# Kernel tuning notes

Hardware: AMD Instinct MI355X
Metric: run time of the kernel (lower is better)

## Reference

```python
import jax, jax.numpy as jnp
import numpy as np

STEP_SIZE = 0.3333
MAX_STEPS = 8          # >= ceil(max(2*sigma)/step); extra iterations have k==0 (no-op)
TANGENT_DIRECTION = True


def _bilinear_sample(img, p):
    # img: [B,C,H,W], p: [B,2,H,W] normalized coords in [0,1] (x=width, y=height)
    B, C, H, W = img.shape
    fx = p[:, 0] * W - 0.5   # [B,H,W] pixel-center convention
    fy = p[:, 1] * H - 0.5
    x0 = jnp.floor(fx)
    y0 = jnp.floor(fy)
    wx = (fx - x0)[:, None]  # [B,1,H,W]
    wy = (fy - y0)[:, None]
    x0i = jnp.clip(x0.astype(jnp.int32), 0, W - 1)
    x1i = jnp.clip(x0i + 1, 0, W - 1)
    y0i = jnp.clip(y0.astype(jnp.int32), 0, H - 1)
    y1i = jnp.clip(y0i + 1, 0, H - 1)
    gather = jax.vmap(lambda im, yi, xi: im[:, yi, xi])  # per-batch gather -> [B,C,H,W]
    v00 = gather(img, y0i, x0i)
    v01 = gather(img, y0i, x1i)
    v10 = gather(img, y1i, x0i)
    v11 = gather(img, y1i, x1i)
    return (v00 * (1 - wx) + v01 * wx) * (1 - wy) + (v10 * (1 - wx) + v11 * wx) * wy


def _p_start(H, W, dtype):
    xs = (jnp.arange(W, dtype=dtype) + 0.5) / W
    ys = (jnp.arange(H, dtype=dtype) + 0.5) / H
    px = jnp.broadcast_to(xs[None, :], (H, W))
    py = jnp.broadcast_to(ys[:, None], (H, W))
    return jnp.stack([px, py])[None]  # [1,2,H,W]


def _perp(t):
    return jnp.concatenate([t[:, 1:2], -t[:, 0:1]], axis=1)


def _forward(x, tangent, sigma):
    B, C, H, W = x.shape
    dt = x.dtype
    factor = min(H, W) / 1024.0          # input_size_factor relative to 1024 base res
    sigma = sigma * factor               # [B,1,1,1]
    half_width = 2.0 * sigma
    two_sigma2 = 2.0 * sigma * sigma
    step = jnp.asarray(1.0 / (STEP_SIZE * factor), dtype=dt)
    tex = jnp.array([W, H], dtype=dt).reshape(1, 2, 1, 1)
    p0 = _p_start(H, W, dt)

    def one_pass(direction):
        v = direction if TANGENT_DIRECTION else _perp(direction)
        p = p0 + v / tex
        r = jnp.broadcast_to(step, (B, 1, 1, 1))
        c = jnp.zeros_like(x)
        s = jnp.zeros((B, 1, H, W), dt)

        def body(carry, _):
            c, s, v, p, r = carry
            k = jnp.exp(-r * r / two_sigma2)                 # [B,1,1,1]
            k = jnp.where(r < half_width, k, 0.0)
            inb = ((p[:, 0:1] >= 0.0) & (p[:, 0:1] < 1.0) &
                   (p[:, 1:2] >= 0.0) & (p[:, 1:2] < 1.0))   # [B,1,H,W]
            k = jnp.where(inb, k, 0.0)                        # [B,1,H,W]
            c = c + _bilinear_sample(x, p) * k
            s = s + k
            tf = _bilinear_sample(tangent, p)                 # [B,2,H,W]
            if not TANGENT_DIRECTION:
                tf = _perp(tf)
            vt = jnp.sum(v * tf, axis=1, keepdims=True)
            tf = jnp.where(vt < 0.0, -tf, tf)                 # keep marching direction coherent
            return (c, s, tf, p + tf / tex, r + step), None

        (c, s, _, _, _), _ = jax.lax.scan(body, (c, s, v, p, r), None, length=MAX_STEPS)
        return c, s

    c1, s1 = one_pass(tangent)
    c2, s2 = one_pass(-tangent)
    return (x + c1 + c2) / (1.0 + s1 + s2)


def setup_inputs() -> dict:
    key = jax.random.key(0)
    k1, k2, k3 = jax.random.split(key, 3)
    B, C, H, W = 2, 3, 1024, 1024
    x = jax.random.uniform(k1, (B, C, H, W), dtype=jnp.float32)
    t = jax.random.normal(k2, (B, 2, H, W), dtype=jnp.float32)
    t = t / (jnp.sqrt(jnp.sum(t * t, axis=1, keepdims=True)) + 1e-6)  # unit tangent field
    sigma = 2.0 + 4.0 * jax.random.uniform(k3, (B, 1, 1, 1), dtype=jnp.float32)
    return {"x": x, "tangent": t, "sigma": sigma}


def reference(x, tangent, sigma):
    return _forward(x, tangent, sigma)
```

## Files before the change

kernel.cpp:

```cpp
#include <hip/hip_runtime.h>
#include <hip/hip_fp16.h>


#define HH 1024
#define WW 1024
#define CC 3
#define BB 2
#define NPIX (HH * WW)

#define TSX 16
#define TSY 16
#define HALO_LO 4
#define NWIN 25

__device__ __forceinline__ float uaf(unsigned u) { return __uint_as_float(u); }
__device__ __forceinline__ __half2 h2(unsigned u) {
    __half2 r; *(unsigned*)&r = u; return r;
}

__global__ __launch_bounds__(256) void flow_smooth_lds(
    const float* __restrict__ x, const float* __restrict__ tng,
    const float* __restrict__ sigma, float* __restrict__ out)
{
    __shared__ float2 tanw[NWIN * NWIN];
    __shared__ uint2  colw[NWIN * NWIN];

    const int id  = (int)blockIdx.x + ((int)blockIdx.y << 6) + ((int)blockIdx.z << 12);
    const int swz = ((id & 7) << 10) + (id >> 3);
    const int bx = swz & 63;
    const int by = (swz >> 6) & 63;
    const int b  = swz >> 12;

    const int tile_x0 = bx * TSX;
    const int tile_y0 = by * TSY;
    const int win_x0 = tile_x0 - HALO_LO;
    const int win_y0 = tile_y0 - HALO_LO;
    const bool border = (bx == 0) | (bx == 63) | (by == 0) | (by == 63);

    const float* __restrict__ xb  = x   + (size_t)b * CC * NPIX;
    const float* __restrict__ tbx = tng + (size_t)b * 2 * NPIX;
    const float* __restrict__ tby = tbx + NPIX;

    if (!border) {
        const int gbase = win_y0 * WW + win_x0;
        for (unsigned j = threadIdx.x; j < NWIN * NWIN; j += 256) {
            const int jy = (int)(j / NWIN);
            const int jx = (int)j - jy * NWIN;
            const int g = gbase + (jy << 10) + jx;
            tanw[j] = make_float2(tbx[g], tby[g]);
            const __half2 c01 = __floats2half2_rn(xb[g], xb[NPIX + g]);
            const __half2 c2p = __floats2half2_rn(xb[2 * NPIX + g], 0.f);
            uint2 r;
            r.x = *(const unsigned*)&c01;
            r.y = *(const unsigned*)&c2p;
            colw[j] = r;
        }
    } else {
        for (unsigned j = threadIdx.x; j < NWIN * NWIN; j += 256) {
            const int jy = (int)(j / NWIN);
            const int jx = (int)j - jy * NWIN;
            const int gy = min(max(win_y0 + jy, 0), HH - 1);
            const int gx = min(max(win_x0 + jx, 0), WW - 1);
            const int g = gy * WW + gx;
            tanw[j] = make_float2(tbx[g], tby[g]);
            const __half2 c01 = __floats2half2_rn(xb[g], xb[NPIX + g]);
            const __half2 c2p = __floats2half2_rn(xb[2 * NPIX + g], 0.f);
            uint2 r;
            r.x = *(const unsigned*)&c01;
            r.y = *(const unsigned*)&c2p;
            colw[j] = r;
        }
    }
    __syncthreads();

    const int tx = threadIdx.x & (TSX - 1);
    const int ty = threadIdx.x >> 4;
    const int ix = tile_x0 + tx;
    const int iy = tile_y0 + ty;
    const int pix = iy * WW + ix;

    const float sig = sigma[b];
    const float half_width = 2.0f * sig;
    const float inv2s2 = 1.0f / (2.0f * sig * sig);
    const float step = (float)(1.0 / 0.3333);

    const float r0 = step;
    const float r1 = r0 + step;
    const float r2 = r1 + step;
    const int nlive = (int)(r0 < half_width) + (int)(r1 < half_width) + (int)(r2 < half_width);
    const float kk0 = __expf(-r0 * r0 * inv2s2);
    const float kk1 = __expf(-r1 * r1 * inv2s2);
    const float kk2 = __expf(-r2 * r2 * inv2s2);

    const float xc0 = xb[pix];
    const float xc1 = xb[NPIX + pix];
    const float xc2 = xb[2 * NPIX + pix];
    const int cidx = (ty + HALO_LO) * NWIN + (tx + HALO_LO);
    const float2 tc = tanw[cidx];
    const float t0x = tc.x;
    const float t0y = tc.y;

    const float invW = 1.0f / WW;
    const float invH = 1.0f / HH;

    float acc0 = 0.f, acc1 = 0.f, acc2 = 0.f, accs = 0.f;

    float vx[2], vy[2], px[2], py[2];
    vx[0] = t0x;  vy[0] = t0y;
    vx[1] = -t0x; vy[1] = -t0y;
    const float p0x = ((float)ix + 0.5f) * invW;
    const float p0y = ((float)iy + 0.5f) * invH;
    px[0] = p0x + vx[0] * invW;  py[0] = p0y + vy[0] * invH;
    px[1] = p0x + vx[1] * invW;  py[1] = p0y + vy[1] * invH;

    if (!border) {
        const int winoff = win_y0 * NWIN + win_x0;
        #pragma unroll
        for (int it = 0; it < 3; ++it) {
            if (it >= nlive) break;
            const float k = (it == 0) ? kk0 : (it == 1) ? kk1 : kk2;
            const bool need_t = (it + 1 < nlive);
            #pragma unroll
            for (int c = 0; c < 2; ++c) {
                const float fx = fmaf(px[c], (float)WW, -0.5f);
                const float fy = fmaf(py[c], (float)HH, -0.5f);
                const float x0f = floorf(fx);
                const float y0f = floorf(fy);
                const float wx = fx - x0f;
                const float wy = fy - y0f;
                const int idx = (int)y0f * NWIN + (int)x0f - winoff;

                const float wxm = 1.f - wx, wym = 1.f - wy;
                const float w00 = wxm * wym, w01 = wx * wym;
                const float w10 = wxm * wy,  w11 = wx * wy;

                const uint2 q00 = colw[idx];
                const uint2 q01 = colw[idx + 1];
                const uint2 q10 = colw[idx + NWIN];
                const uint2 q11 = colw[idx + NWIN + 1];
                const __half2 h00 = __float2half2_rn(w00);
                const __half2 h01 = __float2half2_rn(w01);
                const __half2 h10 = __float2half2_rn(w10);
                const __half2 h11 = __float2half2_rn(w11);
                __half2 a01 = __hmul2(h00, h2(q00.x));
                a01 = __hfma2(h01, h2(q01.x), a01);
                a01 = __hfma2(h10, h2(q10.x), a01);
                a01 = __hfma2(h11, h2(q11.x), a01);
                __half2 a2 = __hmul2(h00, h2(q00.y));
                a2 = __hfma2(h01, h2(q01.y), a2);
                a2 = __hfma2(h10, h2(q10.y), a2);
                a2 = __hfma2(h11, h2(q11.y), a2);
                acc0 = fmaf(k, __low2float(a01), acc0);
                acc1 = fmaf(k, __high2float(a01), acc1);
                acc2 = fmaf(k, __low2float(a2), acc2);

                if (need_t) {
                    const float2 t00 = tanw[idx];
                    const float2 t01 = tanw[idx + 1];
                    const float2 t10 = tanw[idx + NWIN];
                    const float2 t11 = tanw[idx + NWIN + 1];
                    float tfx = t00.x * w00 + t01.x * w01 + t10.x * w10 + t11.x * w11;
                    float tfy = t00.y * w00 + t01.y * w01 + t10.y * w10 + t11.y * w11;
                    const float vt = vx[c] * tfx + vy[c] * tfy;
                    const unsigned sgn = __float_as_uint(vt) & 0x80000000u;
                    tfx = __uint_as_float(__float_as_uint(tfx) ^ sgn);
                    tfy = __uint_as_float(__float_as_uint(tfy) ^ sgn);
                    vx[c] = tfx; vy[c] = tfy;
                    px[c] += tfx * invW;
                    py[c] += tfy * invH;
                }
            }
        }
        float ks = 0.f;
        if (nlive > 0) ks += kk0;
        if (nlive > 1) ks += kk1;
        if (nlive > 2) ks += kk2;
        accs = 2.0f * ks;
    } else {
        #pragma unroll
        for (int it = 0; it < 3; ++it) {
            if (it >= nlive) break;
            const float k = (it == 0) ? kk0 : (it == 1) ? kk1 : kk2;
            #pragma unroll
            for (int c = 0; c < 2; ++c) {
                const float fx = fmaf(px[c], (float)WW, -0.5f);
                const float fy = fmaf(py[c], (float)HH, -0.5f);
                const float x0f = floorf(fx);
                const float y0f = floorf(fy);
                const float wx = fx - x0f;
                const float wy = fy - y0f;
                int x0i = (int)x0f;
                int y0i = (int)y0f;
                x0i = min(max(x0i, 0), WW - 1);
                y0i = min(max(y0i, 0), HH - 1);
                const int x1i = min(x0i + 1, WW - 1);
                const int y1i = min(y0i + 1, HH - 1);

                const int jx0 = x0i - win_x0;
                const int jx1 = x1i - win_x0;
                const int jy0 = y0i - win_y0;
                const int jy1 = y1i - win_y0;
                const int i00 = jy0 * NWIN + jx0;
                const int i01 = jy0 * NWIN + jx1;
                const int i10 = jy1 * NWIN + jx0;
                const int i11 = jy1 * NWIN + jx1;

                const float wxm = 1.f - wx, wym = 1.f - wy;
                const float w00 = wxm * wym, w01 = wx * wym;
                const float w10 = wxm * wy,  w11 = wx * wy;

                const bool inb = (px[c] >= 0.f) & (px[c] < 1.f) &
                                 (py[c] >= 0.f) & (py[c] < 1.f);
                const float kg = inb ? k : 0.f;

                const uint2 q00 = colw[i00];
                const uint2 q01 = colw[i01];
                const uint2 q10 = colw[i10];
                const uint2 q11 = colw[i11];
                const __half2 h00 = __float2half2_rn(w00);
                const __half2 h01 = __float2half2_rn(w01);
                const __half2 h10 = __float2half2_rn(w10);
                const __half2 h11 = __float2half2_rn(w11);
                __half2 a01 = __hmul2(h00, h2(q00.x));
                a01 = __hfma2(h01, h2(q01.x), a01);
                a01 = __hfma2(h10, h2(q10.x), a01);
                a01 = __hfma2(h11, h2(q11.x), a01);
                __half2 a2 = __hmul2(h00, h2(q00.y));
                a2 = __hfma2(h01, h2(q01.y), a2);
                a2 = __hfma2(h10, h2(q10.y), a2);
                a2 = __hfma2(h11, h2(q11.y), a2);
                acc0 = fmaf(kg, __low2float(a01), acc0);
                acc1 = fmaf(kg, __high2float(a01), acc1);
                acc2 = fmaf(kg, __low2float(a2), acc2);
                accs += kg;

                const float2 t00 = tanw[i00];
                const float2 t01 = tanw[i01];
                const float2 t10 = tanw[i10];
                const float2 t11 = tanw[i11];
                float tfx = t00.x * w00 + t01.x * w01 + t10.x * w10 + t11.x * w11;
                float tfy = t00.y * w00 + t01.y * w01 + t10.y * w10 + t11.y * w11;
                const float vt = vx[c] * tfx + vy[c] * tfy;
                const unsigned sgn = __float_as_uint(vt) & 0x80000000u;
                tfx = __uint_as_float(__float_as_uint(tfx) ^ sgn);
                tfy = __uint_as_float(__float_as_uint(tfy) ^ sgn);
                vx[c] = tfx; vy[c] = tfy;
                px[c] += tfx * invW;
                py[c] += tfy * invH;
            }
        }
    }

    const float inv_den = 1.0f / (1.0f + accs);
    float* ob = out + (size_t)b * CC * NPIX;
    ob[pix]            = (xc0 + acc0) * inv_den;
    ob[NPIX + pix]     = (xc1 + acc1) * inv_den;
    ob[2 * NPIX + pix] = (xc2 + acc2) * inv_den;
}

extern "C" void kernel_launch(void* const* d_in, const int* in_sizes, int n_in,
                              void* d_out, int out_size, void* d_ws, size_t ws_size,
                              hipStream_t stream) {
    const float* x  = (const float*)d_in[0];
    const float* t  = (const float*)d_in[1];
    const float* sg = (const float*)d_in[2];
    float* out = (float*)d_out;

    dim3 grid(WW / TSX, HH / TSY, BB);
    flow_smooth_lds<<<grid, dim3(256), 0, stream>>>(x, t, sg, out);
}
```

Measured before the change: 108.4 us.

## Widen tile to 32x16 with two pixels per thread to cut halo overhead

Each 256-thread block now covers a 32x16 tile, with every thread handling two pixels 16 columns apart. The shared window becomes 41x25 instead of 25x25, which lowers the halo load cost per output pixel and halves the block count. In exchange each thread holds more registers and the block uses more LDS, which may reduce occupancy. Each thread also has two independent chains, giving more instruction-level parallelism.

```diff
diff --git a/kernel.cpp b/kernel.cpp
--- a/kernel.cpp
+++ b/kernel.cpp
@@ -8,12 +8,13 @@
 #define BB 2
 #define NPIX (HH * WW)
 
-#define TSX 16
+#define TSX 32
 #define TSY 16
 #define HALO_LO 4
-#define NWIN 25
-
-__device__ __forceinline__ float uaf(unsigned u) { return __uint_as_float(u); }
+#define NWX 41
+#define NWY 25
+#define NREC (NWX * NWY)
+
 __device__ __forceinline__ __half2 h2(unsigned u) {
     __half2 r; *(unsigned*)&r = u; return r;
 }
@@ -22,20 +23,20 @@
     const float* __restrict__ x, const float* __restrict__ tng,
     const float* __restrict__ sigma, float* __restrict__ out)
 {
-    __shared__ float2 tanw[NWIN * NWIN];
-    __shared__ uint2  colw[NWIN * NWIN];
-
-    const int id  = (int)blockIdx.x + ((int)blockIdx.y << 6) + ((int)blockIdx.z << 12);
-    const int swz = ((id & 7) << 10) + (id >> 3);
-    const int bx = swz & 63;
-    const int by = (swz >> 6) & 63;
-    const int b  = swz >> 12;
+    __shared__ float2 tanw[NREC];
+    __shared__ uint2  colw[NREC];
+
+    const int id  = (int)blockIdx.x + ((int)blockIdx.y << 5) + ((int)blockIdx.z << 11);
+    const int swz = ((id & 7) << 9) + (id >> 3);
+    const int bx = swz & 31;
+    const int by = (swz >> 5) & 63;
+    const int b  = swz >> 11;
 
     const int tile_x0 = bx * TSX;
     const int tile_y0 = by * TSY;
     const int win_x0 = tile_x0 - HALO_LO;
     const int win_y0 = tile_y0 - HALO_LO;
-    const bool border = (bx == 0) | (bx == 63) | (by == 0) | (by == 63);
+    const bool border = (bx == 0) | (bx == 31) | (by == 0) | (by == 63);
 
     const float* __restrict__ xb  = x   + (size_t)b * CC * NPIX;
     const float* __restrict__ tbx = tng + (size_t)b * 2 * NPIX;
@@ -43,9 +44,9 @@
 
     if (!border) {
         const int gbase = win_y0 * WW + win_x0;
-        for (unsigned j = threadIdx.x; j < NWIN * NWIN; j += 256) {
-            const int jy = (int)(j / NWIN);
-            const int jx = (int)j - jy * NWIN;
+        for (unsigned j = threadIdx.x; j < NREC; j += 256) {
+            const int jy = (int)(j / NWX);
+            const int jx = (int)j - jy * NWX;
             const int g = gbase + (jy << 10) + jx;
             tanw[j] = make_float2(tbx[g], tby[g]);
             const __half2 c01 = __floats2half2_rn(xb[g], xb[NPIX + g]);
@@ -56,9 +57,9 @@
             colw[j] = r;
         }
     } else {
-        for (unsigned j = threadIdx.x; j < NWIN * NWIN; j += 256) {
-            const int jy = (int)(j / NWIN);
-            const int jx = (int)j - jy * NWIN;
+        for (unsigned j = threadIdx.x; j < NREC; j += 256) {
+            const int jy = (int)(j / NWX);
+            const int jx = (int)j - jy * NWX;
             const int gy = min(max(win_y0 + jy, 0), HH - 1);
             const int gx = min(max(win_x0 + jx, 0), WW - 1);
             const int g = gy * WW + gx;
@@ -73,11 +74,9 @@
     }
     __syncthreads();
 
-    const int tx = threadIdx.x & (TSX - 1);
+    const int tx = threadIdx.x & 15;
     const int ty = threadIdx.x >> 4;
-    const int ix = tile_x0 + tx;
     const int iy = tile_y0 + ty;
-    const int pix = iy * WW + ix;
 
     const float sig = sigma[b];
     const float half_width = 2.0f * sig;
@@ -92,82 +91,90 @@
     const float kk1 = __expf(-r1 * r1 * inv2s2);
     const float kk2 = __expf(-r2 * r2 * inv2s2);
 
-    const float xc0 = xb[pix];
-    const float xc1 = xb[NPIX + pix];
-    const float xc2 = xb[2 * NPIX + pix];
-    const int cidx = (ty + HALO_LO) * NWIN + (tx + HALO_LO);
-    const float2 tc = tanw[cidx];
-    const float t0x = tc.x;
-    const float t0y = tc.y;
-
     const float invW = 1.0f / WW;
     const float invH = 1.0f / HH;
 
-    float acc0 = 0.f, acc1 = 0.f, acc2 = 0.f, accs = 0.f;
-
-    float vx[2], vy[2], px[2], py[2];
-    vx[0] = t0x;  vy[0] = t0y;
-    vx[1] = -t0x; vy[1] = -t0y;
-    const float p0x = ((float)ix + 0.5f) * invW;
-    const float p0y = ((float)iy + 0.5f) * invH;
-    px[0] = p0x + vx[0] * invW;  py[0] = p0y + vy[0] * invH;
-    px[1] = p0x + vx[1] * invW;  py[1] = p0y + vy[1] * invH;
+    int   ix[2], pix[2];
+    float xc0[2], xc1[2], xc2[2];
+    float acc0[2] = {0.f, 0.f}, acc1[2] = {0.f, 0.f};
+    float acc2[2] = {0.f, 0.f}, accs[2] = {0.f, 0.f};
+    float vx[2][2], vy[2][2], px[2][2], py[2][2];
+
+    #pragma unroll
+    for (int pp = 0; pp < 2; ++pp) {
+        ix[pp] = tile_x0 + tx + pp * 16;
+        pix[pp] = iy * WW + ix[pp];
+        xc0[pp] = xb[pix[pp]];
+        xc1[pp] = xb[NPIX + pix[pp]];
+        xc2[pp] = xb[2 * NPIX + pix[pp]];
+        const int cidx = (ty + HALO_LO) * NWX + (tx + pp * 16 + HALO_LO);
+        const float2 tc = tanw[cidx];
+        vx[pp][0] = tc.x;  vy[pp][0] = tc.y;
+        vx[pp][1] = -tc.x; vy[pp][1] = -tc.y;
+        const float p0x = ((float)ix[pp] + 0.5f) * invW;
+        const float p0y = ((float)iy + 0.5f) * invH;
+        px[pp][0] = p0x + vx[pp][0] * invW;  py[pp][0] = p0y + vy[pp][0] * invH;
+        px[pp][1] = p0x + vx[pp][1] * invW;  py[pp][1] = p0y + vy[pp][1] * invH;
+    }
 
     if (!border) {
-        const int winoff = win_y0 * NWIN + win_x0;
+        const int winoff = win_y0 * NWX + win_x0;
         #pragma unroll
         for (int it = 0; it < 3; ++it) {
             if (it >= nlive) break;
             const float k = (it == 0) ? kk0 : (it == 1) ? kk1 : kk2;
             const bool need_t = (it + 1 < nlive);
             #pragma unroll
-            for (int c = 0; c < 2; ++c) {
-                const float fx = fmaf(px[c], (float)WW, -0.5f);
-                const float fy = fmaf(py[c], (float)HH, -0.5f);
-                const float x0f = floorf(fx);
-                const float y0f = floorf(fy);
-                const float wx = fx - x0f;
-                const float wy = fy - y0f;
-                const int idx = (int)y0f * NWIN + (int)x0f - winoff;
-
-                const float wxm = 1.f - wx, wym = 1.f - wy;
-                const float w00 = wxm * wym, w01 = wx * wym;
-                const float w10 = wxm * wy,  w11 = wx * wy;
-
-                const uint2 q00 = colw[idx];
-                const uint2 q01 = colw[idx + 1];
-                const uint2 q10 = colw[idx + NWIN];
-                const uint2 q11 = colw[idx + NWIN + 1];
-                const __half2 h00 = __float2half2_rn(w00);
-                const __half2 h01 = __float2half2_rn(w01);
-                const __half2 h10 = __float2half2_rn(w10);
-                const __half2 h11 = __float2half2_rn(w11);
-                __half2 a01 = __hmul2(h00, h2(q00.x));
-                a01 = __hfma2(h01, h2(q01.x), a01);
-                a01 = __hfma2(h10, h2(q10.x), a01);
-                a01 = __hfma2(h11, h2(q11.x), a01);
-                __half2 a2 = __hmul2(h00, h2(q00.y));
-                a2 = __hfma2(h01, h2(q01.y), a2);
-                a2 = __hfma2(h10, h2(q10.y), a2);
-                a2 = __hfma2(h11, h2(q11.y), a2);
-                acc0 = fmaf(k, __low2float(a01), acc0);
-                acc1 = fmaf(k, __high2float(a01), acc1);
-                acc2 = fmaf(k, __low2float(a2), acc2);
-
-                if (need_t) {
-                    const float2 t00 = tanw[idx];
-                    const float2 t01 = tanw[idx + 1];
-                    const float2 t10 = tanw[idx + NWIN];
-                    const float2 t11 = tanw[idx + NWIN + 1];
-                    float tfx = t00.x * w00 + t01.x * w01 + t10.x * w10 + t11.x * w11;
-                    float tfy = t00.y * w00 + t01.y * w01 + t10.y * w10 + t11.y * w11;
-                    const float vt = vx[c] * tfx + vy[c] * tfy;
-                    const unsigned sgn = __float_as_uint(vt) & 0x80000000u;
-                    tfx = __uint_as_float(__float_as_uint(tfx) ^ sgn);
-                    tfy = __uint_as_float(__float_as_uint(tfy) ^ sgn);
-                    vx[c] = tfx; vy[c] = tfy;
-                    px[c] += tfx * invW;
-                    py[c] += tfy * invH;
+            for (int pp = 0; pp < 2; ++pp) {
+                #pragma unroll
+                for (int c = 0; c < 2; ++c) {
+                    const float fx = fmaf(px[pp][c], (float)WW, -0.5f);
+                    const float fy = fmaf(py[pp][c], (float)HH, -0.5f);
+                    const float x0f = floorf(fx);
+                    const float y0f = floorf(fy);
+                    const float wx = fx - x0f;
+                    const float wy = fy - y0f;
+                    const int idx = (int)y0f * NWX + (int)x0f - winoff;
+
+                    const float wxm = 1.f - wx, wym = 1.f - wy;
+                    const float w00 = wxm * wym, w01 = wx * wym;
+                    const float w10 = wxm * wy,  w11 = wx * wy;
+
+                    const uint2 q00 = colw[idx];
+                    const uint2 q01 = colw[idx + 1];
+                    const uint2 q10 = colw[idx + NWX];
+                    const uint2 q11 = colw[idx + NWX + 1];
+                    const __half2 h00 = __float2half2_rn(w00);
+                    const __half2 h01 = __float2half2_rn(w01);
+                    const __half2 h10 = __float2half2_rn(w10);
+                    const __half2 h11 = __float2half2_rn(w11);
+                    __half2 a01 = __hmul2(h00, h2(q00.x));
+                    a01 = __hfma2(h01, h2(q01.x), a01);
+                    a01 = __hfma2(h10, h2(q10.x), a01);
+                    a01 = __hfma2(h11, h2(q11.x), a01);
+                    __half2 a2 = __hmul2(h00, h2(q00.y));
+                    a2 = __hfma2(h01, h2(q01.y), a2);
+                    a2 = __hfma2(h10, h2(q10.y), a2);
+                    a2 = __hfma2(h11, h2(q11.y), a2);
+                    acc0[pp] = fmaf(k, __low2float(a01), acc0[pp]);
+                    acc1[pp] = fmaf(k, __high2float(a01), acc1[pp]);
+                    acc2[pp] = fmaf(k, __low2float(a2), acc2[pp]);
+
+                    if (need_t) {
+                        const float2 t00 = tanw[idx];
+                        const float2 t01 = tanw[idx + 1];
+                        const float2 t10 = tanw[idx + NWX];
+                        const float2 t11 = tanw[idx + NWX + 1];
+                        float tfx = t00.x * w00 + t01.x * w01 + t10.x * w10 + t11.x * w11;
+                        float tfy = t00.y * w00 + t01.y * w01 + t10.y * w10 + t11.y * w11;
+                        const float vt = vx[pp][c] * tfx + vy[pp][c] * tfy;
+                        const unsigned sgn = __float_as_uint(vt) & 0x80000000u;
+                        tfx = __uint_as_float(__float_as_uint(tfx) ^ sgn);
+                        tfy = __uint_as_float(__float_as_uint(tfy) ^ sgn);
+                        vx[pp][c] = tfx; vy[pp][c] = tfy;
+                        px[pp][c] += tfx * invW;
+                        py[pp][c] += tfy * invH;
+                    }
                 }
             }
         }
@@ -175,87 +182,94 @@
         if (nlive > 0) ks += kk0;
         if (nlive > 1) ks += kk1;
         if (nlive > 2) ks += kk2;
-        accs = 2.0f * ks;
+        accs[0] = 2.0f * ks;
+        accs[1] = accs[0];
     } else {
         #pragma unroll
         for (int it = 0; it < 3; ++it) {
             if (it >= nlive) break;
             const float k = (it == 0) ? kk0 : (it == 1) ? kk1 : kk2;
             #pragma unroll
-            for (int c = 0; c < 2; ++c) {
-                const float fx = fmaf(px[c], (float)WW, -0.5f);
-                const float fy = fmaf(py[c], (float)HH, -0.5f);
-                const float x0f = floorf(fx);
-                const float y0f = floorf(fy);
-                const float wx = fx - x0f;
-                const float wy = fy - y0f;
-                int x0i = (int)x0f;
-                int y0i = (int)y0f;
-                x0i = min(max(x0i, 0), WW - 1);
-                y0i = min(max(y0i, 0), HH - 1);
-                const int x1i = min(x0i + 1, WW - 1);
-                const int y1i = min(y0i + 1, HH - 1);
-
-                const int jx0 = x0i - win_x0;
-                const int jx1 = x1i - win_x0;
-                const int jy0 = y0i - win_y0;
-                const int jy1 = y1i - win_y0;
-                const int i00 = jy0 * NWIN + jx0;
-                const int i01 = jy0 * NWIN + jx1;
-                const int i10 = jy1 * NWIN + jx0;
-                const int i11 = jy1 * NWIN + jx1;
-
-                const float wxm = 1.f - wx, wym = 1.f - wy;
-                const float w00 = wxm * wym, w01 = wx * wym;
-                const float w10 = wxm * wy,  w11 = wx * wy;
-
-                const bool inb = (px[c] >= 0.f) & (px[c] < 1.f) &
-                                 (py[c] >= 0.f) & (py[c] < 1.f);
-                const float kg = inb ? k : 0.f;
-
-                const uint2 q00 = colw[i00];
-                const uint2 q01 = colw[i01];
-                const uint2 q10 = colw[i10];
-                const uint2 q11 = colw[i11];
-                const __half2 h00 = __float2half2_rn(w00);
-                const __half2 h01 = __float2half2_rn(w01);
-                const __half2 h10 = __float2half2_rn(w10);
-                const __half2 h11 = __float2half2_rn(w11);
-                __half2 a01 = __hmul2(h00, h2(q00.x));
-                a01 = __hfma2(h01, h2(q01.x), a01);
-                a01 = __hfma2(h10, h2(q10.x), a01);
-                a01 = __hfma2(h11, h2(q11.x), a01);
-                __half2 a2 = __hmul2(h00, h2(q00.y));
-                a2 = __hfma2(h01, h2(q01.y), a2);
-                a2 = __hfma2(h10, h2(q10.y), a2);
-                a2 = __hfma2(h11, h2(q11.y), a2);
-                acc0 = fmaf(kg, __low2float(a01), acc0);
-                acc1 = fmaf(kg, __high2float(a01), acc1);
-                acc2 = fmaf(kg, __low2float(a2), acc2);
-                accs += kg;
-
-                const float2 t00 = tanw[i00];
-                const float2 t01 = tanw[i01];
-                const float2 t10 = tanw[i10];
-                const float2 t11 = tanw[i11];
-                float tfx = t00.x * w00 + t01.x * w01 + t10.x * w10 + t11.x * w11;
-                float tfy = t00.y * w00 + t01.y * w01 + t10.y * w10 + t11.y * w11;
-                const float vt = vx[c] * tfx + vy[c] * tfy;
-                const unsigned sgn = __float_as_uint(vt) & 0x80000000u;
-                tfx = __uint_as_float(__float_as_uint(tfx) ^ sgn);
-                tfy = __uint_as_float(__float_as_uint(tfy) ^ sgn);
-                vx[c] = tfx; vy[c] = tfy;
-                px[c] += tfx * invW;
-                py[c] += tfy * invH;
+            for (int pp = 0; pp < 2; ++pp) {
+                #pragma unroll
+                for (int c = 0; c < 2; ++c) {
+                    const float fx = fmaf(px[pp][c], (float)WW, -0.5f);
+                    const float fy = fmaf(py[pp][c], (float)HH, -0.5f);
+                    const float x0f = floorf(fx);
+                    const float y0f = floorf(fy);
+                    const float wx = fx - x0f;
+                    const float wy = fy - y0f;
+                    int x0i = (int)x0f;
+                    int y0i = (int)y0f;
+                    x0i = min(max(x0i, 0), WW - 1);
+                    y0i = min(max(y0i, 0), HH - 1);
+                    const int x1i = min(x0i + 1, WW - 1);
+                    const int y1i = min(y0i + 1, HH - 1);
+
+                    const int jx0 = x0i - win_x0;
+                    const int jx1 = x1i - win_x0;
+                    const int jy0 = y0i - win_y0;
+                    const int jy1 = y1i - win_y0;
+                    const int i00 = jy0 * NWX + jx0;
+                    const int i01 = jy0 * NWX + jx1;
+                    const int i10 = jy1 * NWX + jx0;
+                    const int i11 = jy1 * NWX + jx1;
+
+                    const float wxm = 1.f - wx, wym = 1.f - wy;
+                    const float w00 = wxm * wym, w01 = wx * wym;
+                    const float w10 = wxm * wy,  w11 = wx * wy;
+
+                    const bool inb = (px[pp][c] >= 0.f) & (px[pp][c] < 1.f) &
+                                     (py[pp][c] >= 0.f) & (py[pp][c] < 1.f);
+                    const float kg = inb ? k : 0.f;
+
+                    const uint2 q00 = colw[i00];
+                    const uint2 q01 = colw[i01];
+                    const uint2 q10 = colw[i10];
+                    const uint2 q11 = colw[i11];
+                    const __half2 h00 = __float2half2_rn(w00);
+                    const __half2 h01 = __float2half2_rn(w01);
+                    const __half2 h10 = __float2half2_rn(w10);
+                    const __half2 h11 = __float2half2_rn(w11);
+                    __half2 a01 = __hmul2(h00, h2(q00.x));
+                    a01 = __hfma2(h01, h2(q01.x), a01);
+                    a01 = __hfma2(h10, h2(q10.x), a01);
+                    a01 = __hfma2(h11, h2(q11.x), a01);
+                    __half2 a2 = __hmul2(h00, h2(q00.y));
+                    a2 = __hfma2(h01, h2(q01.y), a2);
+                    a2 = __hfma2(h10, h2(q10.y), a2);
+                    a2 = __hfma2(h11, h2(q11.y), a2);
+                    acc0[pp] = fmaf(kg, __low2float(a01), acc0[pp]);
+                    acc1[pp] = fmaf(kg, __high2float(a01), acc1[pp]);
+                    acc2[pp] = fmaf(kg, __low2float(a2), acc2[pp]);
+                    accs[pp] += kg;
+
+                    const float2 t00 = tanw[i00];
+                    const float2 t01 = tanw[i01];
+                    const float2 t10 = tanw[i10];
+                    const float2 t11 = tanw[i11];
+                    float tfx = t00.x * w00 + t01.x * w01 + t10.x * w10 + t11.x * w11;
+                    float tfy = t00.y * w00 + t01.y * w01 + t10.y * w10 + t11.y * w11;
+                    const float vt = vx[pp][c] * tfx + vy[pp][c] * tfy;
+                    const unsigned sgn = __float_as_uint(vt) & 0x80000000u;
+                    tfx = __uint_as_float(__float_as_uint(tfx) ^ sgn);
+                    tfy = __uint_as_float(__float_as_uint(tfy) ^ sgn);
+                    vx[pp][c] = tfx; vy[pp][c] = tfy;
+                    px[pp][c] += tfx * invW;
+                    py[pp][c] += tfy * invH;
+                }
             }
         }
     }
 
-    const float inv_den = 1.0f / (1.0f + accs);
     float* ob = out + (size_t)b * CC * NPIX;
-    ob[pix]            = (xc0 + acc0) * inv_den;
-    ob[NPIX + pix]     = (xc1 + acc1) * inv_den;
-    ob[2 * NPIX + pix] = (xc2 + acc2) * inv_den;
+    #pragma unroll
+    for (int pp = 0; pp < 2; ++pp) {
+        const float inv_den = 1.0f / (1.0f + accs[pp]);
+        ob[pix[pp]]            = (xc0[pp] + acc0[pp]) * inv_den;
+        ob[NPIX + pix[pp]]     = (xc1[pp] + acc1[pp]) * inv_den;
+        ob[2 * NPIX + pix[pp]] = (xc2[pp] + acc2[pp]) * inv_den;
+    }
 }
 
 extern "C" void kernel_launch(void* const* d_in, const int* in_sizes, int n_in,
```

Measured after the change: 111.0 us. 2.4% more time.
